# Kernel optimization log

Measured on AMD Instinct MI355X. Metric: run time of the kernel, lower is better.

The kernel has to match this reference:

```python
import jax, jax.numpy as jnp
import numpy as np

B, C, H, W = 4, 192, 128, 128
GAMMA = 0.9
HIDDEN = int(C * 2.66)  # 510
EPS_NORM = 1e-12
EPS_LN = 1e-5


def conv2d(x, w, b, groups=1, pad=0):
    # x: (B,Cin,H,W), w: (Cout, Cin//groups, kh, kw)
    y = jax.lax.conv_general_dilated(
        x, w, window_strides=(1, 1), padding=[(pad, pad), (pad, pad)],
        dimension_numbers=("NCHW", "OIHW", "NCHW"), feature_group_count=groups)
    return y + b[None, :, None, None]


def setup_inputs() -> dict:
    key = jax.random.key(0)
    ks = jax.random.split(key, 32)
    s = 0.02
    d = {
        "Q": jax.random.normal(ks[0], (B, C, H, W), jnp.float32),
        "Fn": jax.random.normal(ks[1], (B, C, H, W), jnp.float32),
        "temperature": jnp.ones((1,), jnp.float32),
        # q/k/v projections: 1x1 conv then depthwise 3x3
        "qw1": jax.random.normal(ks[2], (C, C, 1, 1)) * s, "qb1": jnp.zeros((C,)),
        "qw2": jax.random.normal(ks[3], (C, 1, 3, 3)) * s, "qb2": jnp.zeros((C,)),
        "kw1": jax.random.normal(ks[4], (C, C, 1, 1)) * s, "kb1": jnp.zeros((C,)),
        "kw2": jax.random.normal(ks[5], (C, 1, 3, 3)) * s, "kb2": jnp.zeros((C,)),
        "vw1": jax.random.normal(ks[6], (C, C, 1, 1)) * s, "vb1": jnp.zeros((C,)),
        "vw2": jax.random.normal(ks[7], (C, 1, 3, 3)) * s, "vb2": jnp.zeros((C,)),
        "ow": jax.random.normal(ks[8], (C, C, 1, 1)) * s, "ob": jnp.zeros((C,)),
        # LayerNorm over channels
        "ln_w": jnp.ones((C,)), "ln_b": jnp.zeros((C,)),
        # FFN: proj_in 1x1 -> 2*HIDDEN, dw 3x3 (groups=2*HIDDEN), proj_out HIDDEN -> C
        "fi_w": jax.random.normal(ks[9], (2 * HIDDEN, C, 1, 1)) * s, "fi_b": jnp.zeros((2 * HIDDEN,)),
        "fd_w": jax.random.normal(ks[10], (2 * HIDDEN, 1, 3, 3)) * s, "fd_b": jnp.zeros((2 * HIDDEN,)),
        "fo_w": jax.random.normal(ks[11], (C, HIDDEN, 1, 1)) * s, "fo_b": jnp.zeros((C,)),
    }
    return {k: v.astype(jnp.float32) for k, v in d.items()}


def _forward(Q, Fn, temperature, qw1, qb1, qw2, qb2, kw1, kb1, kw2, kb2,
             vw1, vb1, vw2, vb2, ow, ob, ln_w, ln_b, fi_w, fi_b, fd_w, fd_b, fo_w, fo_b):
    q = conv2d(conv2d(Q, qw1, qb1), qw2, qb2, groups=C, pad=1).reshape(B, C, H * W)
    k = conv2d(conv2d(Fn, kw1, kb1), kw2, kb2, groups=C, pad=1).reshape(B, C, H * W)
    v = conv2d(conv2d(Fn, vw1, vb1), vw2, vb2, groups=C, pad=1).reshape(B, C, H * W)
    # L2 normalize along spatial (last) dim
    q = q / jnp.maximum(jnp.linalg.norm(q, axis=-1, keepdims=True), EPS_NORM)
    k = k / jnp.maximum(jnp.linalg.norm(k, axis=-1, keepdims=True), EPS_NORM)
    attn = jnp.einsum("bcn,bdn->bcd", q, k) * temperature  # (B,C,C)
    attn = jax.nn.softmax(attn, axis=-1)
    k_keep = max(1, int(C * GAMMA))
    topk_vals, _ = jax.lax.top_k(attn, k_keep)
    threshold = topk_vals[:, :, -1:]
    attn = attn * (attn >= threshold).astype(attn.dtype)
    out = jnp.einsum("bcd,bdn->bcn", attn, v).reshape(B, C, H, W)
    Fa = conv2d(out, ow, ob)
    # LayerNorm over channel dim (per pixel)
    xp = Fa.transpose(0, 2, 3, 1)  # (B,H,W,C)
    mu = xp.mean(-1, keepdims=True)
    var = ((xp - mu) ** 2).mean(-1, keepdims=True)
    xn = ((xp - mu) / jnp.sqrt(var + EPS_LN)) * ln_w + ln_b
    xn = xn.transpose(0, 3, 1, 2)
    # FFN
    h = conv2d(xn, fi_w, fi_b)
    h = conv2d(h, fd_w, fd_b, groups=2 * HIDDEN, pad=1)
    x1, x2 = h[:, :HIDDEN], h[:, HIDDEN:]
    h = x1 * jax.nn.gelu(x2, approximate=False)
    ffn_out = conv2d(h, fo_w, fo_b)
    return Fa + ffn_out


def reference(Q, Fn, temperature, qw1, qb1, qw2, qb2, kw1, kb1, kw2, kb2,
              vw1, vb1, vw2, vb2, ow, ob, ln_w, ln_b, fi_w, fi_b, fd_w, fd_b, fo_w, fo_b):
    return _forward(Q, Fn, temperature, qw1, qb1, qw2, qb2, kw1, kb1, kw2, kb2,
                    vw1, vb1, vw2, vb2, ow, ob, ln_w, ln_b, fi_w, fi_b, fd_w, fd_b, fo_w, fo_b)
```

## Files before the change

### kernel.cpp

```cpp
#include <hip/hip_runtime.h>
#include <math.h>
#include <float.h>

#define NPIX 16384
#define CC 192
#define BB 4
#define HHH 128
#define WWW 128
#define HID 510
#define HID2 1020
#define KKEEP 172
#define KSPLIT 16

typedef unsigned short ushort;
typedef unsigned int uint32;
using f32x4  = __attribute__((ext_vector_type(4))) float;
using bf16x8 = __attribute__((ext_vector_type(8))) short;

__device__ __forceinline__ float bf2f(ushort u) {
  union { float f; unsigned int i; } x; x.i = ((unsigned int)u) << 16; return x.f;
}
__device__ __forceinline__ ushort f2bf(float f) {
  union { float f; unsigned int i; } x; x.f = f;
  unsigned int r = (x.i + 0x7FFFu + ((x.i >> 16) & 1u)) >> 16;
  return (ushort)r;
}

struct __align__(16) us8 { ushort u[8]; };
struct __align__(8)  us4 { ushort u[4]; };

__global__ __launch_bounds__(256) void k_wconv(
    const float* __restrict__ fiw, const float* __restrict__ fow,
    ushort* __restrict__ fiwb, ushort* __restrict__ fowb)
{
  const int idx = blockIdx.x * 256 + threadIdx.x;
  if (idx < 1024 * 192) {
    const int r = idx / 192, c = idx % 192;
    fiwb[idx] = (r < HID2) ? f2bf(fiw[r * 192 + c]) : (ushort)0;
  }
  const int i2 = idx - 1024 * 192;
  if (i2 >= 0 && i2 < 192 * 512) {
    const int r = i2 / 512, c = i2 % 512;
    fowb[i2] = (c < HID) ? f2bf(fow[r * HID + c]) : (ushort)0;
  }
}

__global__ __launch_bounds__(256) void k_tsplit(
    const float* __restrict__ X, ushort* __restrict__ Xh, ushort* __restrict__ Xl)
{
  __shared__ float ld[64][261];
  const int b = blockIdx.z;
  const int c0 = blockIdx.y * 64;
  const int px0 = blockIdx.x * 256;
  const int tid = threadIdx.x;
  #pragma unroll
  for (int i = 0; i < 16; ++i) {
    const int u = i * 256 + tid;
    const int r = u >> 6, p4 = (u & 63) * 4;
    const float4 v = *reinterpret_cast<const float4*>(
        X + ((size_t)b * CC + c0 + r) * NPIX + px0 + p4);
    ld[r][p4] = v.x; ld[r][p4 + 1] = v.y; ld[r][p4 + 2] = v.z; ld[r][p4 + 3] = v.w;
  }
  __syncthreads();
  const int c8 = (tid & 7) * 8;
  #pragma unroll
  for (int it = 0; it < 8; ++it) {
    const int pl = it * 32 + (tid >> 3);
    us8 hi, lo;
    #pragma unroll
    for (int j = 0; j < 8; ++j) {
      const float v = ld[c8 + j][pl];
      const ushort h = f2bf(v);
      hi.u[j] = h; lo.u[j] = f2bf(v - bf2f(h));
    }
    const size_t off = ((size_t)b * NPIX + px0 + pl) * CC + c0 + c8;
    *reinterpret_cast<us8*>(Xh + off) = hi;
    *reinterpret_cast<us8*>(Xl + off) = lo;
  }
}

__global__ __launch_bounds__(256) void k_nt3res(
    const float* __restrict__ W,
    const ushort* __restrict__ Bh, const ushort* __restrict__ Bl,
    const float* __restrict__ bias, float* __restrict__ C,
    long long sAb)
{
  __shared__ ushort As[2][64][200];
  __shared__ ushort Bs[2][128][200];
  const int b = blockIdx.z;
  const int n0 = blockIdx.x * 128;
  const int m0 = blockIdx.y * 64;
  const int tid = threadIdx.x;
  const int lane = tid & 63;
  const int wave = tid >> 6;
  const int wm = wave >> 1, wn = wave & 1;
  const float*  Wb  = W  + (size_t)b * sAb;
  const ushort* Bhb = Bh + (size_t)b * NPIX * CC;
  const ushort* Blb = Bl + (size_t)b * NPIX * CC;

  #pragma unroll
  for (int i = 0; i < 12; ++i) {
    const int u = i * 256 + tid;
    const int r = u / 48, c = (u % 48) * 4;
    const float4 v = *reinterpret_cast<const float4*>(Wb + (size_t)(m0 + r) * CC + c);
    const float e[4] = {v.x, v.y, v.z, v.w};
    us4 hi, lo;
    #pragma unroll
    for (int t = 0; t < 4; ++t) {
      const ushort h = f2bf(e[t]);
      hi.u[t] = h; lo.u[t] = f2bf(e[t] - bf2f(h));
    }
    *reinterpret_cast<us4*>(&As[0][r][c]) = hi;
    *reinterpret_cast<us4*>(&As[1][r][c]) = lo;
  }
  #pragma unroll
  for (int i = 0; i < 12; ++i) {
    const int u = i * 256 + tid;
    const int r = u / 24, c = (u % 24) * 8;
    *reinterpret_cast<us8*>(&Bs[0][r][c]) =
        *reinterpret_cast<const us8*>(Bhb + (size_t)(n0 + r) * CC + c);
    *reinterpret_cast<us8*>(&Bs[1][r][c]) =
        *reinterpret_cast<const us8*>(Blb + (size_t)(n0 + r) * CC + c);
  }
  __syncthreads();

  f32x4 acc[2][4];
  #pragma unroll
  for (int i = 0; i < 2; ++i)
    #pragma unroll
    for (int j = 0; j < 4; ++j) acc[i][j] = (f32x4){0.f, 0.f, 0.f, 0.f};

  #pragma unroll
  for (int kk = 0; kk < 6; ++kk) {
    bf16x8 af[2][2], bfg[4][2];
    #pragma unroll
    for (int mi = 0; mi < 2; ++mi)
      #pragma unroll
      for (int p = 0; p < 2; ++p)
        af[mi][p] = *reinterpret_cast<const bf16x8*>(
            &As[p][wm * 32 + mi * 16 + (lane & 15)][kk * 32 + (lane >> 4) * 8]);
    #pragma unroll
    for (int ni = 0; ni < 4; ++ni)
      #pragma unroll
      for (int p = 0; p < 2; ++p)
        bfg[ni][p] = *reinterpret_cast<const bf16x8*>(
            &Bs[p][wn * 64 + ni * 16 + (lane & 15)][kk * 32 + (lane >> 4) * 8]);
    #pragma unroll
    for (int mi = 0; mi < 2; ++mi)
      #pragma unroll
      for (int ni = 0; ni < 4; ++ni) {
        acc[mi][ni] = __builtin_amdgcn_mfma_f32_16x16x32_bf16(
            af[mi][0], bfg[ni][0], acc[mi][ni], 0, 0, 0);
        acc[mi][ni] = __builtin_amdgcn_mfma_f32_16x16x32_bf16(
            af[mi][0], bfg[ni][1], acc[mi][ni], 0, 0, 0);
        acc[mi][ni] = __builtin_amdgcn_mfma_f32_16x16x32_bf16(
            af[mi][1], bfg[ni][0], acc[mi][ni], 0, 0, 0);
      }
  }

  #pragma unroll
  for (int mi = 0; mi < 2; ++mi)
    #pragma unroll
    for (int r = 0; r < 4; ++r) {
      const int m = m0 + wm * 32 + mi * 16 + (lane >> 4) * 4 + r;
      const float bv = bias[m];
      #pragma unroll
      for (int ni = 0; ni < 4; ++ni) {
        const int n = n0 + wn * 64 + ni * 16 + (lane & 15);
        C[(size_t)b * CC * NPIX + (size_t)m * NPIX + n] = acc[mi][ni][r] + bv;
      }
    }
}

__global__ __launch_bounds__(256) void k_fi(
    const ushort* __restrict__ Aw, const ushort* __restrict__ Bt,
    const float* __restrict__ bias, ushort* __restrict__ H)
{
  __shared__ ushort As[128][200];
  __shared__ ushort Bs[128][200];
  __shared__ ushort Cs[64][132];
  const int z = blockIdx.z;
  const int n0 = blockIdx.x * 128;
  const int m0 = blockIdx.y * 128;
  const int tid = threadIdx.x;
  const int lane = tid & 63;
  const int wave = tid >> 6;
  const int wm = wave >> 1, wn = wave & 1;
  const ushort* Bb = Bt + (size_t)z * NPIX * CC;
  ushort* Hb = H + (size_t)z * 1024 * NPIX;

  #pragma unroll
  for (int i = 0; i < 12; ++i) {
    const int u = i * 256 + tid;
    const int r = u / 24, c = (u % 24) * 8;
    *reinterpret_cast<us8*>(&As[r][c]) =
        *reinterpret_cast<const us8*>(Aw + (size_t)(m0 + r) * CC + c);
    *reinterpret_cast<us8*>(&Bs[r][c]) =
        *reinterpret_cast<const us8*>(Bb + (size_t)(n0 + r) * CC + c);
  }
  __syncthreads();

  f32x4 acc[4][4];
  #pragma unroll
  for (int i = 0; i < 4; ++i)
    #pragma unroll
    for (int j = 0; j < 4; ++j) acc[i][j] = (f32x4){0.f, 0.f, 0.f, 0.f};

  #pragma unroll
  for (int kk = 0; kk < 6; ++kk) {
    bf16x8 af[4], bfg[4];
    #pragma unroll
    for (int mi = 0; mi < 4; ++mi)
      af[mi] = *reinterpret_cast<const bf16x8*>(
          &As[wm * 64 + mi * 16 + (lane & 15)][kk * 32 + (lane >> 4) * 8]);
    #pragma unroll
    for (int ni = 0; ni < 4; ++ni)
      bfg[ni] = *reinterpret_cast<const bf16x8*>(
          &Bs[wn * 64 + ni * 16 + (lane & 15)][kk * 32 + (lane >> 4) * 8]);
    #pragma unroll
    for (int mi = 0; mi < 4; ++mi)
      #pragma unroll
      for (int ni = 0; ni < 4; ++ni)
        acc[mi][ni] = __builtin_amdgcn_mfma_f32_16x16x32_bf16(
            af[mi], bfg[ni], acc[mi][ni], 0, 0, 0);
  }

  #pragma unroll
  for (int half = 0; half < 2; ++half) {
    if (wm == half) {
      #pragma unroll
      for (int mi = 0; mi < 4; ++mi)
        #pragma unroll
        for (int rr = 0; rr < 4; ++rr) {
          const int rloc = mi * 16 + (lane >> 4) * 4 + rr;
          const int m = m0 + half * 64 + rloc;
          const float bv = (m < HID2) ? bias[m] : 0.f;
          #pragma unroll
          for (int ni = 0; ni < 4; ++ni) {
            const int cc = wn * 64 + ni * 16 + (lane & 15);
            Cs[rloc][cc] = f2bf(acc[mi][ni][rr] + bv);
          }
        }
    }
    __syncthreads();
    #pragma unroll
    for (int it = 0; it < 4; ++it) {
      const int r = it * 16 + (tid >> 4);
      const int c8 = (tid & 15) * 8;
      const int m = m0 + half * 64 + r;
      *reinterpret_cast<us8*>(Hb + (size_t)m * NPIX + n0 + c8) =
          *reinterpret_cast<const us8*>(&Cs[r][c8]);
    }
    __syncthreads();
  }
}

__global__ __launch_bounds__(256) void k_fo(
    const ushort* __restrict__ Aw, const ushort* __restrict__ Bt,
    const float* __restrict__ bias, const float* __restrict__ res,
    float* __restrict__ C)
{
  __shared__ ushort As[64][520];
  __shared__ ushort Bs[2][128][136];
  const int z = blockIdx.z;
  const int n0 = blockIdx.x * 128;
  const int m0 = blockIdx.y * 64;
  const int tid = threadIdx.x;
  const int lane = tid & 63;
  const int wave = tid >> 6;
  const int wm = wave >> 1, wn = wave & 1;
  const ushort* Bb = Bt + (size_t)z * NPIX * 512;
  const float* resb = res + (size_t)z * CC * NPIX;
  float* Cb = C + (size_t)z * CC * NPIX;

  #pragma unroll
  for (int i = 0; i < 16; ++i) {
    const int u = i * 256 + tid;
    const int r = u >> 6, c = (u & 63) * 8;
    *reinterpret_cast<us8*>(&As[r][c]) =
        *reinterpret_cast<const us8*>(Aw + (size_t)(m0 + r) * 512 + c);
  }
  #pragma unroll
  for (int i = 0; i < 8; ++i) {
    const int u = i * 256 + tid;
    const int r = u >> 4, c = (u & 15) * 8;
    *reinterpret_cast<us8*>(&Bs[0][r][c]) =
        *reinterpret_cast<const us8*>(Bb + (size_t)(n0 + r) * 512 + c);
  }
  __syncthreads();

  f32x4 acc[2][4];
  #pragma unroll
  for (int i = 0; i < 2; ++i)
    #pragma unroll
    for (int j = 0; j < 4; ++j) acc[i][j] = (f32x4){0.f, 0.f, 0.f, 0.f};

  for (int t = 0; t < 4; ++t) {
    us8 rg[8];
    if (t < 3) {
      #pragma unroll
      for (int i = 0; i < 8; ++i) {
        const int u = i * 256 + tid;
        const int r = u >> 4, c = (u & 15) * 8;
        rg[i] = *reinterpret_cast<const us8*>(
            Bb + (size_t)(n0 + r) * 512 + (t + 1) * 128 + c);
      }
    }
    const int cur = t & 1;
    #pragma unroll
    for (int ks = 0; ks < 4; ++ks) {
      bf16x8 af[2], bfg[4];
      #pragma unroll
      for (int mi = 0; mi < 2; ++mi)
        af[mi] = *reinterpret_cast<const bf16x8*>(
            &As[wm * 32 + mi * 16 + (lane & 15)][t * 128 + ks * 32 + (lane >> 4) * 8]);
      #pragma unroll
      for (int ni = 0; ni < 4; ++ni)
        bfg[ni] = *reinterpret_cast<const bf16x8*>(
            &Bs[cur][wn * 64 + ni * 16 + (lane & 15)][ks * 32 + (lane >> 4) * 8]);
      #pragma unroll
      for (int mi = 0; mi < 2; ++mi)
        #pragma unroll
        for (int ni = 0; ni < 4; ++ni)
          acc[mi][ni] = __builtin_amdgcn_mfma_f32_16x16x32_bf16(
              af[mi], bfg[ni], acc[mi][ni], 0, 0, 0);
    }
    if (t < 3) {
      #pragma unroll
      for (int i = 0; i < 8; ++i) {
        const int u = i * 256 + tid;
        const int r = u >> 4, c = (u & 15) * 8;
        *reinterpret_cast<us8*>(&Bs[cur ^ 1][r][c]) = rg[i];
      }
    }
    __syncthreads();
  }

  #pragma unroll
  for (int mi = 0; mi < 2; ++mi)
    #pragma unroll
    for (int r = 0; r < 4; ++r) {
      const int m = m0 + wm * 32 + mi * 16 + (lane >> 4) * 4 + r;
      const float bv = bias[m];
      #pragma unroll
      for (int ni = 0; ni < 4; ++ni) {
        const int n = n0 + wn * 64 + ni * 16 + (lane & 15);
        Cb[(size_t)m * NPIX + n] = acc[mi][ni][r] + bv + resb[(size_t)m * NPIX + n];
      }
    }
}

__global__ __launch_bounds__(256) void k_attn_mfma(
    const ushort* __restrict__ qh, const ushort* __restrict__ ql,
    const ushort* __restrict__ kh, const ushort* __restrict__ kl,
    float* __restrict__ part)
{
  __shared__ ushort As[2][64][40];
  __shared__ ushort Bs[2][64][40];
  const int b = blockIdx.z;
  const int tr = blockIdx.x / 3, tc = blockIdx.x % 3;
  const int r0 = tr * 64, c0 = tc * 64;
  const int k0 = blockIdx.y * (NPIX / KSPLIT);
  const int tid = threadIdx.x;
  const int lane = tid & 63;
  const int wave = tid >> 6;
  const int wm = wave >> 1, wn = wave & 1;

  f32x4 acc[2][2];
  #pragma unroll
  for (int i = 0; i < 2; ++i)
    #pragma unroll
    for (int j = 0; j < 2; ++j) acc[i][j] = (f32x4){0.f, 0.f, 0.f, 0.f};

  const int ar = tid >> 2, ak = (tid & 3) * 8;

  for (int kc = 0; kc < NPIX / KSPLIT; kc += 32) {
    const size_t qo = (size_t)(b * CC + r0 + ar) * NPIX + k0 + kc + ak;
    const size_t ko = (size_t)(b * CC + c0 + ar) * NPIX + k0 + kc + ak;
    *reinterpret_cast<us8*>(&As[0][ar][ak]) = *reinterpret_cast<const us8*>(qh + qo);
    *reinterpret_cast<us8*>(&As[1][ar][ak]) = *reinterpret_cast<const us8*>(ql + qo);
    *reinterpret_cast<us8*>(&Bs[0][ar][ak]) = *reinterpret_cast<const us8*>(kh + ko);
    *reinterpret_cast<us8*>(&Bs[1][ar][ak]) = *reinterpret_cast<const us8*>(kl + ko);
    __syncthreads();
    bf16x8 af[2][2], bfr[2][2];
    #pragma unroll
    for (int mi = 0; mi < 2; ++mi)
      #pragma unroll
      for (int p = 0; p < 2; ++p)
        af[mi][p] = *reinterpret_cast<const bf16x8*>(
            &As[p][wm * 32 + mi * 16 + (lane & 15)][(lane >> 4) * 8]);
    #pragma unroll
    for (int ni = 0; ni < 2; ++ni)
      #pragma unroll
      for (int p = 0; p < 2; ++p)
        bfr[ni][p] = *reinterpret_cast<const bf16x8*>(
            &Bs[p][wn * 32 + ni * 16 + (lane & 15)][(lane >> 4) * 8]);
    #pragma unroll
    for (int mi = 0; mi < 2; ++mi)
      #pragma unroll
      for (int ni = 0; ni < 2; ++ni) {
        acc[mi][ni] = __builtin_amdgcn_mfma_f32_16x16x32_bf16(
            af[mi][0], bfr[ni][0], acc[mi][ni], 0, 0, 0);
        acc[mi][ni] = __builtin_amdgcn_mfma_f32_16x16x32_bf16(
            af[mi][0], bfr[ni][1], acc[mi][ni], 0, 0, 0);
        acc[mi][ni] = __builtin_amdgcn_mfma_f32_16x16x32_bf16(
            af[mi][1], bfr[ni][0], acc[mi][ni], 0, 0, 0);
      }
    __syncthreads();
  }

  float* pp = part + (size_t)(blockIdx.y * BB + b) * CC * CC;
  #pragma unroll
  for (int mi = 0; mi < 2; ++mi)
    #pragma unroll
    for (int r = 0; r < 4; ++r) {
      const int row = r0 + wm * 32 + mi * 16 + (lane >> 4) * 4 + r;
      #pragma unroll
      for (int ni = 0; ni < 2; ++ni) {
        const int col = c0 + wn * 32 + ni * 16 + (lane & 15);
        pp[(size_t)row * CC + col] = acc[mi][ni][r];
      }
    }
}

__device__ __forceinline__ void dw4(const float* __restrict__ Xc,
                                    const float* __restrict__ wt, float bv,
                                    int h, int w, float out[4])
{
  float a0, a1, a2, a3;
  a0 = a1 = a2 = a3 = bv;
  #pragma unroll
  for (int dy = 0; dy < 3; ++dy) {
    const int hh = h + dy - 1;
    if (hh < 0 || hh >= HHH) continue;
    const float* row = Xc + hh * WWW + w;
    const float xm = (w > 0) ? row[-1] : 0.f;
    const float4 xc = *reinterpret_cast<const float4*>(row);
    const float xp = (w < WWW - 4) ? row[4] : 0.f;
    const float w0 = wt[dy * 3 + 0], w1 = wt[dy * 3 + 1], w2 = wt[dy * 3 + 2];
    a0 += w0 * xm   + w1 * xc.x + w2 * xc.y;
    a1 += w0 * xc.x + w1 * xc.y + w2 * xc.z;
    a2 += w0 * xc.y + w1 * xc.z + w2 * xc.w;
    a3 += w0 * xc.z + w1 * xc.w + w2 * xp;
  }
  out[0] = a0; out[1] = a1; out[2] = a2; out[3] = a3;
}

__global__ __launch_bounds__(256) void k_dw3x3(
    const float* __restrict__ X, const float* __restrict__ W9,
    const float* __restrict__ bias, float* __restrict__ Y)
{
  const int b = blockIdx.z, c = blockIdx.y;
  const int p = blockIdx.x * 1024 + threadIdx.x * 4;
  const int h = p >> 7, w = p & 127;
  float o[4];
  dw4(X + (size_t)(b * CC + c) * NPIX, W9 + c * 9, bias[c], h, w, o);
  *reinterpret_cast<float4*>(Y + (size_t)(b * CC + c) * NPIX + p) =
      make_float4(o[0], o[1], o[2], o[3]);
}

__global__ __launch_bounds__(256) void k_dw3x3_split(
    const float* __restrict__ X, const float* __restrict__ W9,
    const float* __restrict__ bias, ushort* __restrict__ Yh,
    ushort* __restrict__ Yl)
{
  const int b = blockIdx.z, c = blockIdx.y;
  const int p = blockIdx.x * 1024 + threadIdx.x * 4;
  const int h = p >> 7, w = p & 127;
  float o[4];
  dw4(X + (size_t)(b * CC + c) * NPIX, W9 + c * 9, bias[c], h, w, o);
  us4 hi, lo;
  #pragma unroll
  for (int t = 0; t < 4; ++t) {
    const ushort hv = f2bf(o[t]);
    hi.u[t] = hv;
    lo.u[t] = f2bf(o[t] - bf2f(hv));
  }
  const size_t off = (size_t)(b * CC + c) * NPIX + p;
  *reinterpret_cast<us4*>(Yh + off) = hi;
  *reinterpret_cast<us4*>(Yl + off) = lo;
}

__global__ __launch_bounds__(256) void k_rownorm2(
    const ushort* __restrict__ qh, const ushort* __restrict__ ql,
    const ushort* __restrict__ kh, const ushort* __restrict__ kl,
    float* __restrict__ rq, float* __restrict__ rk)
{
  const int row = blockIdx.x;
  const ushort* H = blockIdx.y ? kh : qh;
  const ushort* L = blockIdx.y ? kl : ql;
  float* R = blockIdx.y ? rk : rq;
  const ushort* Hr = H + (size_t)row * NPIX;
  const ushort* Lr = L + (size_t)row * NPIX;
  float s = 0.f;
  for (int i = threadIdx.x * 8; i < NPIX; i += 2048) {
    const us8 a = *reinterpret_cast<const us8*>(Hr + i);
    const us8 bb = *reinterpret_cast<const us8*>(Lr + i);
    #pragma unroll
    for (int t = 0; t < 8; ++t) {
      const float v = bf2f(a.u[t]) + bf2f(bb.u[t]);
      s += v * v;
    }
  }
  __shared__ float sm[256];
  sm[threadIdx.x] = s; __syncthreads();
  for (int st = 128; st > 0; st >>= 1) {
    if (threadIdx.x < st) sm[threadIdx.x] += sm[threadIdx.x + st];
    __syncthreads();
  }
  if (threadIdx.x == 0) R[row] = 1.f / fmaxf(sqrtf(sm[0]), 1e-12f);
}

__global__ __launch_bounds__(192) void k_softmax_topk(
    const float* __restrict__ part, const float* __restrict__ rq,
    const float* __restrict__ rk, const float* __restrict__ temp,
    float* __restrict__ attnm)
{
  const int c = blockIdx.x, b = blockIdx.y, d = threadIdx.x;
  float s = 0.f;
  for (int ksp = 0; ksp < KSPLIT; ++ksp)
    s += part[(size_t)(ksp * BB + b) * CC * CC + c * CC + d];
  const float logit = s * rq[b * CC + c] * rk[b * CC + d] * temp[0];
  __shared__ float sa[CC], sb[CC];
  sa[d] = logit; __syncthreads();
  float mx = -FLT_MAX;
  for (int j = 0; j < CC; ++j) mx = fmaxf(mx, sa[j]);
  const float e = expf(logit - mx);
  sb[d] = e; __syncthreads();
  float sum = 0.f;
  for (int j = 0; j < CC; ++j) sum += sb[j];
  const float pv = e / sum;
  __syncthreads();
  sa[d] = pv; __syncthreads();
  int greater = 0;
  for (int j = 0; j < CC; ++j) greater += (sa[j] > pv) ? 1 : 0;
  const float cand = (greater < KKEEP) ? pv : FLT_MAX;
  sb[d] = cand; __syncthreads();
  float thr = FLT_MAX;
  for (int j = 0; j < CC; ++j) thr = fminf(thr, sb[j]);
  attnm[(size_t)(b * CC + c) * CC + d] = (pv >= thr) ? pv : 0.f;
}

__global__ __launch_bounds__(192) void k_mix(
    const float* __restrict__ ow, const float* __restrict__ attnm,
    float* __restrict__ M)
{
  const int c = blockIdx.x, b = blockIdx.y, d = threadIdx.x;
  float acc = 0.f;
  for (int e = 0; e < CC; ++e)
    acc += ow[c * CC + e] * attnm[(size_t)(b * CC + e) * CC + d];
  M[(size_t)(b * CC + c) * CC + d] = acc;
}

__global__ __launch_bounds__(256) void k_ln_t(
    const float* __restrict__ X, const float* __restrict__ lw,
    const float* __restrict__ lb, ushort* __restrict__ Y)
{
  const int b = blockIdx.y;
  const int n = blockIdx.x * 256 + threadIdx.x;
  const float* Xb = X + (size_t)b * CC * NPIX + n;
  float s = 0.f, s2 = 0.f;
  for (int ci = 0; ci < CC; ++ci) {
    const float v = Xb[(size_t)ci * NPIX];
    s += v; s2 += v * v;
  }
  const float mu = s * (1.f / CC);
  const float var = fmaxf(s2 * (1.f / CC) - mu * mu, 0.f);
  const float rstd = rsqrtf(var + 1e-5f);
  ushort* Yb = Y + ((size_t)b * NPIX + n) * CC;
  for (int c8 = 0; c8 < CC / 8; ++c8) {
    bf16x8 sv;
    #pragma unroll
    for (int t = 0; t < 8; ++t) {
      const int c = c8 * 8 + t;
      const float v = Xb[(size_t)c * NPIX];
      sv[t] = (short)f2bf((v - mu) * rstd * lw[c] + lb[c]);
    }
    *reinterpret_cast<bf16x8*>(Yb + c8 * 8) = sv;
  }
}

__device__ __forceinline__ float gelu_exact(float x) {
  return 0.5f * x * (1.f + erff(x * 0.70710678118654752f));
}

__global__ __launch_bounds__(256) void k_dwglu3(
    const ushort* __restrict__ Hp, const float* __restrict__ fdw,
    const float* __restrict__ fdb, ushort* __restrict__ gt)
{
  __shared__ ushort hs[16][4][128];
  __shared__ uint32 gsd[8 * 129];
  const int z = blockIdx.z;
  const int c0 = blockIdx.x * 8;
  const int h0 = blockIdx.y * 2;
  const int tid = threadIdx.x;
  const int npairs = min(8, HID - c0);
  const ushort* Hb = Hp + (size_t)z * 1024 * NPIX;

  #pragma unroll
  for (int i = 0; i < 4; ++i) {
    const int u = i * 256 + tid;
    const int ch = u >> 6;
    const int row = (u >> 4) & 3;
    const int w0 = (u & 15) * 8;
    const int grow = h0 - 1 + row;
    const int cloc = ch & 7;
    const int gch = (ch < 8) ? (c0 + cloc) : (HID + c0 + cloc);
    us8 v;
    #pragma unroll
    for (int t = 0; t < 8; ++t) v.u[t] = 0;
    if (c0 + cloc < HID && grow >= 0 && grow < HHH)
      v = *reinterpret_cast<const us8*>(Hb + (size_t)gch * NPIX + grow * WWW + w0);
    *reinterpret_cast<us8*>(&hs[ch][row][w0]) = v;
  }
  __syncthreads();

  const int q = tid & 63;
  const int jp = tid >> 6;
  const int px_l = q * 4;
  const int dh = px_l >> 7;
  const int w = px_l & 127;

  #pragma unroll
  for (int jj = 0; jj < 2; ++jj) {
    const int j = jp * 2 + jj;
    uint32 p0 = 0, p1 = 0;
    if (j < npairs) {
      const float* w1 = fdw + (size_t)(c0 + j) * 9;
      const float* w2 = fdw + (size_t)(HID + c0 + j) * 9;
      float x1[4], x2[4];
      const float b1 = fdb[c0 + j], b2 = fdb[HID + c0 + j];
      #pragma unroll
      for (int i = 0; i < 4; ++i) { x1[i] = b1; x2[i] = b2; }
      #pragma unroll
      for (int dy = 0; dy < 3; ++dy) {
        const int row = dh + dy;
        const ushort* r1 = &hs[j][row][0];
        const ushort* r2 = &hs[8 + j][row][0];
        const float am1 = (w > 0) ? bf2f(r1[w - 1]) : 0.f;
        const float am2 = (w > 0) ? bf2f(r2[w - 1]) : 0.f;
        const us4 c1 = *reinterpret_cast<const us4*>(&r1[w]);
        const us4 c2 = *reinterpret_cast<const us4*>(&r2[w]);
        const float ap1 = (w < 124) ? bf2f(r1[w + 4]) : 0.f;
        const float ap2 = (w < 124) ? bf2f(r2[w + 4]) : 0.f;
        const float e10 = bf2f(c1.u[0]), e11 = bf2f(c1.u[1]);
        const float e12 = bf2f(c1.u[2]), e13 = bf2f(c1.u[3]);
        const float e20 = bf2f(c2.u[0]), e21 = bf2f(c2.u[1]);
        const float e22 = bf2f(c2.u[2]), e23 = bf2f(c2.u[3]);
        const float wa0 = w1[dy * 3 + 0], wa1 = w1[dy * 3 + 1], wa2 = w1[dy * 3 + 2];
        const float wb0 = w2[dy * 3 + 0], wb1 = w2[dy * 3 + 1], wb2 = w2[dy * 3 + 2];
        x1[0] += wa0 * am1 + wa1 * e10 + wa2 * e11;
        x1[1] += wa0 * e10 + wa1 * e11 + wa2 * e12;
        x1[2] += wa0 * e11 + wa1 * e12 + wa2 * e13;
        x1[3] += wa0 * e12 + wa1 * e13 + wa2 * ap1;
        x2[0] += wb0 * am2 + wb1 * e20 + wb2 * e21;
        x2[1] += wb0 * e20 + wb1 * e21 + wb2 * e22;
        x2[2] += wb0 * e21 + wb1 * e22 + wb2 * e23;
        x2[3] += wb0 * e22 + wb1 * e23 + wb2 * ap2;
      }
      const ushort v0 = f2bf(x1[0] * gelu_exact(x2[0]));
      const ushort v1 = f2bf(x1[1] * gelu_exact(x2[1]));
      const ushort v2 = f2bf(x1[2] * gelu_exact(x2[2]));
      const ushort v3 = f2bf(x1[3] * gelu_exact(x2[3]));
      p0 = (uint32)v0 | ((uint32)v1 << 16);
      p1 = (uint32)v2 | ((uint32)v3 << 16);
    }
    gsd[j * 129 + (px_l >> 1)] = p0;
    gsd[j * 129 + (px_l >> 1) + 1] = p1;
  }
  __syncthreads();

  const ushort* gsu = (const ushort*)gsd;
  const int px_l2 = tid;
  const int px = (h0 + (px_l2 >> 7)) * WWW + (px_l2 & 127);
  us8 v;
  #pragma unroll
  for (int t = 0; t < 8; ++t) v.u[t] = gsu[t * 258 + px_l2];
  *reinterpret_cast<us8*>(gt + ((size_t)z * NPIX + px) * 512 + c0) = v;
}

extern "C" void kernel_launch(void* const* d_in, const int* in_sizes, int n_in,
                              void* d_out, int out_size, void* d_ws, size_t ws_size,
                              hipStream_t stream)
{
  const float* Q    = (const float*)d_in[0];
  const float* Fn   = (const float*)d_in[1];
  const float* temp = (const float*)d_in[2];
  const float* qw1  = (const float*)d_in[3];
  const float* qb1  = (const float*)d_in[4];
  const float* qw2  = (const float*)d_in[5];
  const float* qb2  = (const float*)d_in[6];
  const float* kw1  = (const float*)d_in[7];
  const float* kb1  = (const float*)d_in[8];
  const float* kw2  = (const float*)d_in[9];
  const float* kb2  = (const float*)d_in[10];
  const float* vw1  = (const float*)d_in[11];
  const float* vb1  = (const float*)d_in[12];
  const float* vw2  = (const float*)d_in[13];
  const float* vb2  = (const float*)d_in[14];
  const float* ow   = (const float*)d_in[15];
  const float* ob   = (const float*)d_in[16];
  const float* lnw  = (const float*)d_in[17];
  const float* lnb  = (const float*)d_in[18];
  const float* fiw  = (const float*)d_in[19];
  const float* fib  = (const float*)d_in[20];
  const float* fdw  = (const float*)d_in[21];
  const float* fdb  = (const float*)d_in[22];
  const float* fow  = (const float*)d_in[23];
  const float* fob  = (const float*)d_in[24];
  float* out = (float*)d_out;

  char* ws = (char*)d_ws;
  const size_t P = 25165824UL;
  ushort* Qth = (ushort*)(ws + 0 * P);
  ushort* Qtl = (ushort*)(ws + 1 * P);
  ushort* Fth = (ushort*)(ws + 2 * P);
  ushort* Ftl = (ushort*)(ws + 3 * P);
  ushort* qh  = (ushort*)(ws + 4 * P);
  ushort* ql  = (ushort*)(ws + 5 * P);
  ushort* kh  = (ushort*)(ws + 0 * P);
  ushort* kl  = (ushort*)(ws + 1 * P);
  float*  vbuf = (float*)(ws + 2 * P);
  ushort* vth = (ushort*)(ws + 0 * P);
  ushort* vtl = (ushort*)(ws + 1 * P);
  char* smb = ws + 6 * P;
  float* rq    = (float*)(smb);
  float* rk    = (float*)(smb + 4096);
  float* part  = (float*)(smb + 8192);
  float* attnm = (float*)(smb + 8192 + 9437184);
  float* Mm    = (float*)(smb + 8192 + 9437184 + 589824);
  float*  Fa   = (float*)(ws + 4 * P);
  ushort* xnt  = (ushort*)(ws + 0 * P);
  ushort* h2   = (ushort*)(ws + 1 * P);
  ushort* gt2  = (ushort*)(ws + 6 * P);
  ushort* fiwb = (ushort*)(ws + 6 * P + 33554432UL);
  ushort* fowb = (ushort*)(ws + 6 * P + 33554432UL + 393216UL);
  float* bufT = out;

  dim3 blk(256);

  k_wconv<<<dim3(1152), blk, 0, stream>>>(fiw, fow, fiwb, fowb);
  k_tsplit<<<dim3(64, 3, BB), blk, 0, stream>>>(Q,  Qth, Qtl);
  k_tsplit<<<dim3(64, 3, BB), blk, 0, stream>>>(Fn, Fth, Ftl);
  k_nt3res<<<dim3(128, 3, BB), blk, 0, stream>>>(qw1, Qth, Qtl, qb1, bufT, 0);
  k_dw3x3_split<<<dim3(16, CC, BB), blk, 0, stream>>>(bufT, qw2, qb2, qh, ql);
  k_nt3res<<<dim3(128, 3, BB), blk, 0, stream>>>(kw1, Fth, Ftl, kb1, bufT, 0);
  k_dw3x3_split<<<dim3(16, CC, BB), blk, 0, stream>>>(bufT, kw2, kb2, kh, kl);
  k_nt3res<<<dim3(128, 3, BB), blk, 0, stream>>>(vw1, Fth, Ftl, vb1, bufT, 0);
  k_dw3x3<<<dim3(16, CC, BB), blk, 0, stream>>>(bufT, vw2, vb2, vbuf);
  k_rownorm2<<<dim3(BB * CC, 2), blk, 0, stream>>>(qh, ql, kh, kl, rq, rk);
  k_attn_mfma<<<dim3(9, KSPLIT, BB), blk, 0, stream>>>(qh, ql, kh, kl, part);
  k_softmax_topk<<<dim3(CC, BB), dim3(192), 0, stream>>>(part, rq, rk, temp, attnm);
  k_mix<<<dim3(CC, BB), dim3(192), 0, stream>>>(ow, attnm, Mm);
  k_tsplit<<<dim3(64, 3, BB), blk, 0, stream>>>(vbuf, vth, vtl);
  k_nt3res<<<dim3(128, 3, BB), blk, 0, stream>>>(Mm, vth, vtl, ob, Fa,
                                                 (long long)CC * CC);
  k_ln_t<<<dim3(64, BB), blk, 0, stream>>>(Fa, lnw, lnb, xnt);
  for (int p = 0; p < 2; ++p) {
    const ushort* xn_p = xnt + (size_t)(2 * p) * NPIX * CC;
    const float*  fa_p = Fa + (size_t)(2 * p) * CC * NPIX;
    float* out_p = out + (size_t)(2 * p) * CC * NPIX;
    k_fi<<<dim3(128, 8, 2), blk, 0, stream>>>(fiwb, xn_p, fib, h2);
    k_dwglu3<<<dim3(64, 64, 2), blk, 0, stream>>>(h2, fdw, fdb, gt2);
    k_fo<<<dim3(128, 3, 2), blk, 0, stream>>>(fowb, gt2, fob, fa_p, out_p);
  }
}
```

Measured before the change: 713.8 us.

## Fuse K and V 1x1 projections into one launch and shrink FFN-in tile

Adds a kernel that computes both the K and V 1x1 projections of Fn in one launch, with blockIdx.y selecting the weight set, so the Fth/Ftl tiles are read by a single grid instead of two sequential ones. V goes to a temporary buffer and its depthwise conv runs before K's. Separately, k_fi's M tile drops from 128 to 64 and the output staging buffer now aliases the input LDS, cutting shared memory and doubling the grid for more occupancy. The trade-off is that each B tile in k_fi is reloaded twice as often.

New measurement: 652.4 us. 8.6% less time.

```diff
diff --git a/kernel.cpp b/kernel.cpp
--- a/kernel.cpp
+++ b/kernel.cpp
@@ -172,16 +172,113 @@
     }
 }
 
+__global__ __launch_bounds__(256) void k_nt3res2(
+    const float* __restrict__ W1, const float* __restrict__ W2,
+    const ushort* __restrict__ Bh, const ushort* __restrict__ Bl,
+    const float* __restrict__ b1, const float* __restrict__ b2,
+    float* __restrict__ C1, float* __restrict__ C2)
+{
+  __shared__ ushort As[2][64][200];
+  __shared__ ushort Bs[2][128][200];
+  const int b = blockIdx.z;
+  const int n0 = blockIdx.x * 128;
+  const bool sel = blockIdx.y >= 3;
+  const int m0 = (sel ? (blockIdx.y - 3) : blockIdx.y) * 64;
+  const float* W = sel ? W2 : W1;
+  const float* bias = sel ? b2 : b1;
+  float* C = sel ? C2 : C1;
+  const int tid = threadIdx.x;
+  const int lane = tid & 63;
+  const int wave = tid >> 6;
+  const int wm = wave >> 1, wn = wave & 1;
+  const ushort* Bhb = Bh + (size_t)b * NPIX * CC;
+  const ushort* Blb = Bl + (size_t)b * NPIX * CC;
+
+  #pragma unroll
+  for (int i = 0; i < 12; ++i) {
+    const int u = i * 256 + tid;
+    const int r = u / 48, c = (u % 48) * 4;
+    const float4 v = *reinterpret_cast<const float4*>(W + (size_t)(m0 + r) * CC + c);
+    const float e[4] = {v.x, v.y, v.z, v.w};
+    us4 hi, lo;
+    #pragma unroll
+    for (int t = 0; t < 4; ++t) {
+      const ushort h = f2bf(e[t]);
+      hi.u[t] = h; lo.u[t] = f2bf(e[t] - bf2f(h));
+    }
+    *reinterpret_cast<us4*>(&As[0][r][c]) = hi;
+    *reinterpret_cast<us4*>(&As[1][r][c]) = lo;
+  }
+  #pragma unroll
+  for (int i = 0; i < 12; ++i) {
+    const int u = i * 256 + tid;
+    const int r = u / 24, c = (u % 24) * 8;
+    *reinterpret_cast<us8*>(&Bs[0][r][c]) =
+        *reinterpret_cast<const us8*>(Bhb + (size_t)(n0 + r) * CC + c);
+    *reinterpret_cast<us8*>(&Bs[1][r][c]) =
+        *reinterpret_cast<const us8*>(Blb + (size_t)(n0 + r) * CC + c);
+  }
+  __syncthreads();
+
+  f32x4 acc[2][4];
+  #pragma unroll
+  for (int i = 0; i < 2; ++i)
+    #pragma unroll
+    for (int j = 0; j < 4; ++j) acc[i][j] = (f32x4){0.f, 0.f, 0.f, 0.f};
+
+  #pragma unroll
+  for (int kk = 0; kk < 6; ++kk) {
+    bf16x8 af[2][2], bfg[4][2];
+    #pragma unroll
+    for (int mi = 0; mi < 2; ++mi)
+      #pragma unroll
+      for (int p = 0; p < 2; ++p)
+        af[mi][p] = *reinterpret_cast<const bf16x8*>(
+            &As[p][wm * 32 + mi * 16 + (lane & 15)][kk * 32 + (lane >> 4) * 8]);
+    #pragma unroll
+    for (int ni = 0; ni < 4; ++ni)
+      #pragma unroll
+      for (int p = 0; p < 2; ++p)
+        bfg[ni][p] = *reinterpret_cast<const bf16x8*>(
+            &Bs[p][wn * 64 + ni * 16 + (lane & 15)][kk * 32 + (lane >> 4) * 8]);
+    #pragma unroll
+    for (int mi = 0; mi < 2; ++mi)
+      #pragma unroll
+      for (int ni = 0; ni < 4; ++ni) {
+        acc[mi][ni] = __builtin_amdgcn_mfma_f32_16x16x32_bf16(
+            af[mi][0], bfg[ni][0], acc[mi][ni], 0, 0, 0);
+        acc[mi][ni] = __builtin_amdgcn_mfma_f32_16x16x32_bf16(
+            af[mi][0], bfg[ni][1], acc[mi][ni], 0, 0, 0);
+        acc[mi][ni] = __builtin_amdgcn_mfma_f32_16x16x32_bf16(
+            af[mi][1], bfg[ni][0], acc[mi][ni], 0, 0, 0);
+      }
+  }
+
+  #pragma unroll
+  for (int mi = 0; mi < 2; ++mi)
+    #pragma unroll
+    for (int r = 0; r < 4; ++r) {
+      const int m = m0 + wm * 32 + mi * 16 + (lane >> 4) * 4 + r;
+      const float bv = bias[m];
+      #pragma unroll
+      for (int ni = 0; ni < 4; ++ni) {
+        const int n = n0 + wn * 64 + ni * 16 + (lane & 15);
+        C[(size_t)b * CC * NPIX + (size_t)m * NPIX + n] = acc[mi][ni][r] + bv;
+      }
+    }
+}
+
 __global__ __launch_bounds__(256) void k_fi(
     const ushort* __restrict__ Aw, const ushort* __restrict__ Bt,
     const float* __restrict__ bias, ushort* __restrict__ H)
 {
-  __shared__ ushort As[128][200];
-  __shared__ ushort Bs[128][200];
-  __shared__ ushort Cs[64][132];
+  __shared__ ushort lds[64 * 200 + 128 * 200];
+  ushort (*As)[200] = reinterpret_cast<ushort(*)[200]>(lds);
+  ushort (*Bs)[200] = reinterpret_cast<ushort(*)[200]>(lds + 64 * 200);
+  ushort (*Cs)[132] = reinterpret_cast<ushort(*)[132]>(lds);
   const int z = blockIdx.z;
   const int n0 = blockIdx.x * 128;
-  const int m0 = blockIdx.y * 128;
+  const int m0 = blockIdx.y * 64;
   const int tid = threadIdx.x;
   const int lane = tid & 63;
   const int wave = tid >> 6;
@@ -190,68 +287,67 @@
   ushort* Hb = H + (size_t)z * 1024 * NPIX;
 
   #pragma unroll
-  for (int i = 0; i < 12; ++i) {
+  for (int i = 0; i < 6; ++i) {
     const int u = i * 256 + tid;
     const int r = u / 24, c = (u % 24) * 8;
     *reinterpret_cast<us8*>(&As[r][c]) =
         *reinterpret_cast<const us8*>(Aw + (size_t)(m0 + r) * CC + c);
+  }
+  #pragma unroll
+  for (int i = 0; i < 12; ++i) {
+    const int u = i * 256 + tid;
+    const int r = u / 24, c = (u % 24) * 8;
     *reinterpret_cast<us8*>(&Bs[r][c]) =
         *reinterpret_cast<const us8*>(Bb + (size_t)(n0 + r) * CC + c);
   }
   __syncthreads();
 
-  f32x4 acc[4][4];
-  #pragma unroll
-  for (int i = 0; i < 4; ++i)
+  f32x4 acc[2][4];
+  #pragma unroll
+  for (int i = 0; i < 2; ++i)
     #pragma unroll
     for (int j = 0; j < 4; ++j) acc[i][j] = (f32x4){0.f, 0.f, 0.f, 0.f};
 
   #pragma unroll
   for (int kk = 0; kk < 6; ++kk) {
-    bf16x8 af[4], bfg[4];
-    #pragma unroll
-    for (int mi = 0; mi < 4; ++mi)
+    bf16x8 af[2], bfg[4];
+    #pragma unroll
+    for (int mi = 0; mi < 2; ++mi)
       af[mi] = *reinterpret_cast<const bf16x8*>(
-          &As[wm * 64 + mi * 16 + (lane & 15)][kk * 32 + (lane >> 4) * 8]);
+          &As[wm * 32 + mi * 16 + (lane & 15)][kk * 32 + (lane >> 4) * 8]);
     #pragma unroll
     for (int ni = 0; ni < 4; ++ni)
       bfg[ni] = *reinterpret_cast<const bf16x8*>(
           &Bs[wn * 64 + ni * 16 + (lane & 15)][kk * 32 + (lane >> 4) * 8]);
     #pragma unroll
-    for (int mi = 0; mi < 4; ++mi)
+    for (int mi = 0; mi < 2; ++mi)
       #pragma unroll
       for (int ni = 0; ni < 4; ++ni)
         acc[mi][ni] = __builtin_amdgcn_mfma_f32_16x16x32_bf16(
             af[mi], bfg[ni], acc[mi][ni], 0, 0, 0);
   }
 
-  #pragma unroll
-  for (int half = 0; half < 2; ++half) {
-    if (wm == half) {
-      #pragma unroll
-      for (int mi = 0; mi < 4; ++mi)
-        #pragma unroll
-        for (int rr = 0; rr < 4; ++rr) {
-          const int rloc = mi * 16 + (lane >> 4) * 4 + rr;
-          const int m = m0 + half * 64 + rloc;
-          const float bv = (m < HID2) ? bias[m] : 0.f;
-          #pragma unroll
-          for (int ni = 0; ni < 4; ++ni) {
-            const int cc = wn * 64 + ni * 16 + (lane & 15);
-            Cs[rloc][cc] = f2bf(acc[mi][ni][rr] + bv);
-          }
-        }
-    }
-    __syncthreads();
-    #pragma unroll
-    for (int it = 0; it < 4; ++it) {
-      const int r = it * 16 + (tid >> 4);
-      const int c8 = (tid & 15) * 8;
-      const int m = m0 + half * 64 + r;
-      *reinterpret_cast<us8*>(Hb + (size_t)m * NPIX + n0 + c8) =
-          *reinterpret_cast<const us8*>(&Cs[r][c8]);
-    }
-    __syncthreads();
+  __syncthreads();
+  #pragma unroll
+  for (int mi = 0; mi < 2; ++mi)
+    #pragma unroll
+    for (int rr = 0; rr < 4; ++rr) {
+      const int rloc = wm * 32 + mi * 16 + (lane >> 4) * 4 + rr;
+      const int m = m0 + rloc;
+      const float bv = (m < HID2) ? bias[m] : 0.f;
+      #pragma unroll
+      for (int ni = 0; ni < 4; ++ni) {
+        const int cc = wn * 64 + ni * 16 + (lane & 15);
+        Cs[rloc][cc] = f2bf(acc[mi][ni][rr] + bv);
+      }
+    }
+  __syncthreads();
+  #pragma unroll
+  for (int it = 0; it < 4; ++it) {
+    const int r = it * 16 + (tid >> 4);
+    const int c8 = (tid & 15) * 8;
+    *reinterpret_cast<us8*>(Hb + (size_t)(m0 + r) * NPIX + n0 + c8) =
+        *reinterpret_cast<const us8*>(&Cs[r][c8]);
   }
 }
 
@@ -718,9 +814,10 @@
   ushort* Ftl = (ushort*)(ws + 3 * P);
   ushort* qh  = (ushort*)(ws + 4 * P);
   ushort* ql  = (ushort*)(ws + 5 * P);
+  float*  vtmp = (float*)(ws + 0 * P);
+  float*  vbuf = (float*)(ws + 2 * P);
   ushort* kh  = (ushort*)(ws + 0 * P);
   ushort* kl  = (ushort*)(ws + 1 * P);
-  float*  vbuf = (float*)(ws + 2 * P);
   ushort* vth = (ushort*)(ws + 0 * P);
   ushort* vtl = (ushort*)(ws + 1 * P);
   char* smb = ws + 6 * P;
@@ -744,10 +841,10 @@
   k_tsplit<<<dim3(64, 3, BB), blk, 0, stream>>>(Fn, Fth, Ftl);
   k_nt3res<<<dim3(128, 3, BB), blk, 0, stream>>>(qw1, Qth, Qtl, qb1, bufT, 0);
   k_dw3x3_split<<<dim3(16, CC, BB), blk, 0, stream>>>(bufT, qw2, qb2, qh, ql);
-  k_nt3res<<<dim3(128, 3, BB), blk, 0, stream>>>(kw1, Fth, Ftl, kb1, bufT, 0);
+  k_nt3res2<<<dim3(128, 6, BB), blk, 0, stream>>>(kw1, vw1, Fth, Ftl,
+                                                  kb1, vb1, bufT, vtmp);
+  k_dw3x3<<<dim3(16, CC, BB), blk, 0, stream>>>(vtmp, vw2, vb2, vbuf);
   k_dw3x3_split<<<dim3(16, CC, BB), blk, 0, stream>>>(bufT, kw2, kb2, kh, kl);
-  k_nt3res<<<dim3(128, 3, BB), blk, 0, stream>>>(vw1, Fth, Ftl, vb1, bufT, 0);
-  k_dw3x3<<<dim3(16, CC, BB), blk, 0, stream>>>(bufT, vw2, vb2, vbuf);
   k_rownorm2<<<dim3(BB * CC, 2), blk, 0, stream>>>(qh, ql, kh, kl, rq, rk);
   k_attn_mfma<<<dim3(9, KSPLIT, BB), blk, 0, stream>>>(qh, ql, kh, kl, part);
   k_softmax_topk<<<dim3(CC, BB), dim3(192), 0, stream>>>(part, rq, rk, temp, attnm);
@@ -760,7 +857,7 @@
     const ushort* xn_p = xnt + (size_t)(2 * p) * NPIX * CC;
     const float*  fa_p = Fa + (size_t)(2 * p) * CC * NPIX;
     float* out_p = out + (size_t)(2 * p) * CC * NPIX;
-    k_fi<<<dim3(128, 8, 2), blk, 0, stream>>>(fiwb, xn_p, fib, h2);
+    k_fi<<<dim3(128, 16, 2), blk, 0, stream>>>(fiwb, xn_p, fib, h2);
     k_dwglu3<<<dim3(64, 64, 2), blk, 0, stream>>>(h2, fdw, fdb, gt2);
     k_fo<<<dim3(128, 3, 2), blk, 0, stream>>>(fowb, gt2, fob, fa_p, out_p);
   }
```
